# Kernel tuning notes

Measured on AMD Instinct MI355X. Metric: run time of the kernel, lower is better.

The kernel has to match this reference:

```python
import jax, jax.numpy as jnp
import numpy as np

B, DV, W, H = 128, 2048, 14, 14
S = W * H            # 196 spatial positions
DQ = 2048            # question vector dim
DA = 1200            # attention dim_v == dim_q == dim_mm (MLB elementwise fusion)
G = 4                # nb_glimpses
DH = 2048            # fusion dim_h (total); per-glimpse = DH // G
NANS = 3000


def setup_inputs() -> dict:
    key = jax.random.key(0)
    ks = jax.random.split(key, 16)
    s = 0.02
    return {
        "input_v": jax.random.normal(ks[0], (B, DV, W, H), jnp.float32),
        "x_q_vec": jax.random.normal(ks[1], (B, DQ), jnp.float32),
        # conv_v_att: 1x1 conv DV->DA  (expressed as channel matmul)
        "Wv_att": jax.random.normal(ks[2], (DV, DA), jnp.float32) * s,
        "bv_att": jnp.zeros((DA,), jnp.float32),
        # linear_q_att: DQ->DA
        "Wq_att": jax.random.normal(ks[3], (DQ, DA), jnp.float32) * s,
        "bq_att": jnp.zeros((DA,), jnp.float32),
        # conv_att: 1x1 conv DA->G
        "Wa": jax.random.normal(ks[4], (DA, G), jnp.float32) * s,
        "ba": jnp.zeros((G,), jnp.float32),
        # per-glimpse fusion linears DV -> DH//G, stacked over glimpses
        "Wf": jax.random.normal(ks[5], (G, DV, DH // G), jnp.float32) * s,
        "bf": jnp.zeros((G, DH // G), jnp.float32),
        # linear_q_fusion: DQ -> DH
        "Wqf": jax.random.normal(ks[6], (DQ, DH), jnp.float32) * s,
        "bqf": jnp.zeros((DH,), jnp.float32),
        # linear_classif: DH -> NANS
        "Wc": jax.random.normal(ks[7], (DH, NANS), jnp.float32) * s,
        "bc": jnp.zeros((NANS,), jnp.float32),
    }


def reference(input_v, x_q_vec, Wv_att, bv_att, Wq_att, bq_att, Wa, ba,
              Wf, bf, Wqf, bqf, Wc, bc):
    b = input_v.shape[0]
    v_flat = input_v.reshape(b, DV, S)                      # [B, DV, S]

    # --- attention scores ---
    # conv_v_att (1x1) + tanh -> [B, S, DA]
    x_v = jnp.tanh(jnp.einsum('bcs,cd->bsd', v_flat, Wv_att) + bv_att)
    # linear_q_att + tanh -> [B, DA], broadcast over spatial
    x_q = jnp.tanh(x_q_vec @ Wq_att + bq_att)
    # MLB fusion_att: elementwise multiply, then tanh (activation_mm)
    x_att = jnp.tanh(x_v * x_q[:, None, :])                 # [B, S, DA]
    scores = jnp.einsum('bsd,dg->bsg', x_att, Wa) + ba      # [B, S, G]
    att = jax.nn.softmax(scores, axis=1)                    # softmax over spatial

    # --- weighted pooling per glimpse ---
    v_att = jnp.einsum('bsg,bcs->bgc', att, v_flat)         # [B, G, DV]

    # --- fusion of glimpses ---
    xv = jnp.tanh(jnp.einsum('bgc,gch->bgh', v_att, Wf) + bf)  # [B, G, DH/G]
    xv = xv.reshape(b, DH)                                   # concat glimpses
    xq = jnp.tanh(x_q_vec @ Wqf + bqf)                       # [B, DH]
    x = xv * xq                                              # MLB fusion_classif

    # --- classifier ---
    x = jnp.tanh(x)
    return x @ Wc + bc                                       # [B, NANS]
```

## Files before the change

### kernel.cpp

```cpp
#include <hip/hip_runtime.h>
#include <hip/hip_bf16.h>

#define BB   128
#define DV   2048
#define SS   196
#define DQ   2048
#define DA   1200
#define DAP  1280
#define GG   4
#define DH   2048
#define NANS 3000
#define NANSP 3008
#define MROWS (BB*SS)
#define NT   10
#define KSPLIT 8
#define KCHUNK (DV/KSPLIT)
#define NQ   (DAP + DH)

typedef __attribute__((ext_vector_type(8))) short bf16x8;
typedef __attribute__((ext_vector_type(4))) float f32x4;

__device__ __forceinline__ float fast_tanh(float x) {
    float e = __expf(2.0f * x);
    return 1.0f - 2.0f * __builtin_amdgcn_rcpf(e + 1.0f);
}

__device__ __forceinline__ void async_copy16(const void* gsrc, void* ldst) {
    __builtin_amdgcn_global_load_lds(
        (const __attribute__((address_space(1))) void*)gsrc,
        (__attribute__((address_space(3))) void*)ldst, 16, 0, 0);
}

__global__ void pad_misc(const float* __restrict__ bv, const float* __restrict__ Wa,
                         float* __restrict__ bvp, float* __restrict__ wap) {
    int i = blockIdx.x * 256 + threadIdx.x;
    if (i < DAP) bvp[i] = (i < DA) ? bv[i] : 0.f;
    if (i < DAP * GG) {
        int d = i >> 2;
        wap[i] = (d < DA) ? Wa[i] : 0.f;
    }
}

__global__ __launch_bounds__(256) void transpose_v(const float* __restrict__ v,
                                                   __hip_bfloat16* __restrict__ vt) {
    __shared__ float tile[128][65];
    const int b  = blockIdx.z;
    const int c0 = blockIdx.x * 128;
    const int s0 = blockIdx.y * 64;
    const int t  = threadIdx.x;
    const int sl = t & 63;
    const int cr = t >> 6;
    const float* src = v + (size_t)b * DV * SS;
    const int sg = s0 + sl;
    const bool sok = sg < SS;
#pragma unroll
    for (int i = 0; i < 32; ++i) {
        int c = cr + i * 4;
        tile[c][sl] = sok ? src[(size_t)(c0 + c) * SS + sg] : 0.f;
    }
    __syncthreads();
    const int cp = (t & 63) * 2;
#pragma unroll
    for (int i = 0; i < 16; ++i) {
        int s = (t >> 6) + i * 4;
        int sgl = s0 + s;
        if (sgl < SS) {
            __hip_bfloat162 h2;
            h2.x = __float2bfloat16(tile[cp][s]);
            h2.y = __float2bfloat16(tile[cp + 1][s]);
            *(__hip_bfloat162*)(vt + ((size_t)b * SS + sgl) * DV + c0 + cp) = h2;
        }
    }
}

__global__ __launch_bounds__(256) void transpose_w(const float* __restrict__ Wv,
                                                   __hip_bfloat16* __restrict__ wvt) {
    __shared__ float tile[64][65];
    const int d0 = blockIdx.x * 64;
    const int c0 = blockIdx.y * 64;
    const int t  = threadIdx.x;
    const int col  = t & 63;
    const int rowb = t >> 6;
#pragma unroll
    for (int i = 0; i < 16; ++i) {
        int c = rowb + i * 4;
        int d = d0 + col;
        tile[c][col] = (d < DA) ? Wv[(size_t)(c0 + c) * DA + d] : 0.f;
    }
    __syncthreads();
#pragma unroll
    for (int i = 0; i < 16; ++i) {
        int dl = rowb + i * 4;
        wvt[(size_t)(d0 + dl) * DV + c0 + col] = __float2bfloat16(tile[col][dl]);
    }
}

template <int SEL>
__global__ __launch_bounds__(256) void gemm_partial(
    const float* __restrict__ A, int lda,
    const float* __restrict__ Bm, const float* __restrict__ B2,
    float* __restrict__ Cp, int Npad) {
    __shared__ float As[64 * 132];
    __shared__ float Bs[64 * 68];
    const int t     = threadIdx.x;
    const int n0    = blockIdx.x * 64;
    const int kbase = blockIdx.y * KCHUNK;

    const float* Aeff = A;
    const float* Beff;
    int ldb, ncol0, nlim;
    if (SEL == 0) {
        Beff = Bm; ldb = NANS; ncol0 = n0; nlim = NANS;
    } else if (SEL == 1) {
        int gg = n0 >> 9;
        Aeff = A + gg * 2048;
        Beff = Bm + (size_t)gg * 2048 * 512;
        ldb = 512; ncol0 = n0 & 511; nlim = 1 << 30;
    } else {
        if (n0 < DAP) { Beff = Bm; ldb = DA; ncol0 = n0;      nlim = DA; }
        else          { Beff = B2; ldb = DH; ncol0 = n0 - DAP; nlim = 1 << 30; }
    }

    const int tm = (t & 31) * 4;
    const int tn = (t >> 5) * 8;
    float acc[4][8] = {};

    for (int k0 = kbase; k0 < kbase + KCHUNK; k0 += 64) {
        {
            int kk = t & 63, mb = (t >> 6) * 32;
#pragma unroll
            for (int i = 0; i < 32; ++i)
                As[kk * 132 + mb + i] = Aeff[(size_t)(mb + i) * lda + k0 + kk];
        }
        {
            int j = t & 63, kr = t >> 6;
            bool ok = (ncol0 + j) < nlim;
#pragma unroll
            for (int i = 0; i < 16; ++i) {
                int k = kr + i * 4;
                Bs[k * 68 + j] = ok ? Beff[(size_t)(k0 + k) * ldb + ncol0 + j] : 0.f;
            }
        }
        __syncthreads();
#pragma unroll
        for (int kk = 0; kk < 64; ++kk) {
            const float4 av = *(const float4*)(As + kk * 132 + tm);
            const float4 b0 = *(const float4*)(Bs + kk * 68 + tn);
            const float4 b1 = *(const float4*)(Bs + kk * 68 + tn + 4);
            const float am[4] = {av.x, av.y, av.z, av.w};
#pragma unroll
            for (int i = 0; i < 4; ++i) {
                acc[i][0] += am[i] * b0.x; acc[i][1] += am[i] * b0.y;
                acc[i][2] += am[i] * b0.z; acc[i][3] += am[i] * b0.w;
                acc[i][4] += am[i] * b1.x; acc[i][5] += am[i] * b1.y;
                acc[i][6] += am[i] * b1.z; acc[i][7] += am[i] * b1.w;
            }
        }
        __syncthreads();
    }
#pragma unroll
    for (int i = 0; i < 4; ++i) {
        size_t base = ((size_t)blockIdx.y * 128 + tm + i) * Npad + n0 + tn;
        float4 v0 = {acc[i][0], acc[i][1], acc[i][2], acc[i][3]};
        float4 v1 = {acc[i][4], acc[i][5], acc[i][6], acc[i][7]};
        *(float4*)(Cp + base) = v0;
        *(float4*)(Cp + base + 4) = v1;
    }
}

template <int MODE>
__global__ __launch_bounds__(256) void gemm_epilogue(
    const float* __restrict__ Cp, int Npad, int Nreal,
    const float* __restrict__ bias, const float* __restrict__ aux,
    float* __restrict__ out, int ldo) {
    int n = blockIdx.x * 256 + threadIdx.x;
    int m = blockIdx.y;
    if (n >= Npad) return;
    float s = 0.f;
#pragma unroll
    for (int ks = 0; ks < KSPLIT; ++ks)
        s += Cp[((size_t)ks * 128 + m) * Npad + n];
    if (MODE == 0) {
        if (n >= Nreal) return;
        out[(size_t)m * ldo + n] = s + bias[n];
    } else {
        float xv = fast_tanh(s + bias[n]);
        out[(size_t)m * ldo + n] = fast_tanh(xv * aux[(size_t)m * 2048 + n]);
    }
}

__global__ __launch_bounds__(256) void epilogue_q(
    const float* __restrict__ Cp,
    const float* __restrict__ bqa, const float* __restrict__ bqf,
    float* __restrict__ qatt, float* __restrict__ qfus) {
    int n = blockIdx.x * 256 + threadIdx.x;
    int m = blockIdx.y;
    if (n >= NQ) return;
    float s = 0.f;
#pragma unroll
    for (int ks = 0; ks < KSPLIT; ++ks)
        s += Cp[((size_t)ks * 128 + m) * NQ + n];
    if (n < DAP) {
        qatt[(size_t)m * DAP + n] = (n < DA) ? fast_tanh(s + bqa[n]) : 0.f;
    } else {
        int j = n - DAP;
        qfus[(size_t)m * DH + j] = fast_tanh(s + bqf[j]);
    }
}

__global__ __launch_bounds__(256) void big_gemm(
    const __hip_bfloat16* __restrict__ vt,
    const __hip_bfloat16* __restrict__ wt,
    const float* __restrict__ bvp,
    const float* __restrict__ qatt,
    const float* __restrict__ wap,
    float* __restrict__ scores_p) {
    __shared__ __hip_bfloat16 As[128 * 64];
    __shared__ __hip_bfloat16 Bs[128 * 64];
    __shared__ float wa_s[128 * 4];
    __shared__ float sc[128 * 4];
    __shared__ float qs[2 * 128];
    const int t    = threadIdx.x;
    const int lane = t & 63;
    const int w    = t >> 6;
    const int wm   = w >> 1, wn = w & 1;

    int bid = blockIdx.x;
    int grp = bid / 80, r = bid % 80;
    int mt, nt;
    if (grp < 24) { mt = grp * 8 + (r & 7); nt = r >> 3; }
    else          { mt = 192 + (r & 3);     nt = r >> 2; }
    const int m0 = mt * 128, n0 = nt * 128;
    const int b0 = m0 / SS;
    const int b1 = (m0 + 127) / SS;
    const int bsplit = (b0 + 1) * SS;

    if (t < 128) {
        *(float4*)(wa_s + t * 4) = *(const float4*)(wap + (n0 + t) * 4);
        *(float4*)(sc + t * 4) = (float4){0.f, 0.f, 0.f, 0.f};
        qs[t]       = qatt[(size_t)b0 * DAP + n0 + t];
        qs[128 + t] = qatt[(size_t)b1 * DAP + n0 + t];
    }

    f32x4 acc[4][4];
#pragma unroll
    for (int i = 0; i < 4; ++i)
#pragma unroll
        for (int j = 0; j < 4; ++j) acc[i][j] = (f32x4){0.f, 0.f, 0.f, 0.f};

    const int srow   = lane >> 3;
    const int schunk = (lane & 7) ^ srow;
    const __hip_bfloat16* aG = vt + (size_t)(m0 + w * 32 + srow) * DV + schunk * 8;
    const __hip_bfloat16* bG = wt + (size_t)(n0 + w * 32 + srow) * DV + schunk * 8;
    __hip_bfloat16* aL = As + (w * 32) * 64;
    __hip_bfloat16* bL = Bs + (w * 32) * 64;

    for (int k0 = 0; k0 < DV; k0 += 64) {
        __syncthreads();
#pragma unroll
        for (int j = 0; j < 4; ++j) {
            async_copy16(aG + (size_t)(j * 8) * DV + k0, aL + j * 8 * 64);
            async_copy16(bG + (size_t)(j * 8) * DV + k0, bL + j * 8 * 64);
        }
        __syncthreads();
#pragma unroll
        for (int ks = 0; ks < 2; ++ks) {
            const int cx = ((ks * 4 + (lane >> 4)) ^ (lane & 7)) * 8;
            bf16x8 a[4], b[4];
#pragma unroll
            for (int mi = 0; mi < 4; ++mi)
                a[mi] = *(const bf16x8*)(As + (wm * 64 + mi * 16 + (lane & 15)) * 64 + cx);
#pragma unroll
            for (int ni = 0; ni < 4; ++ni)
                b[ni] = *(const bf16x8*)(Bs + (wn * 64 + ni * 16 + (lane & 15)) * 64 + cx);
#pragma unroll
            for (int mi = 0; mi < 4; ++mi)
#pragma unroll
                for (int ni = 0; ni < 4; ++ni)
                    acc[mi][ni] = __builtin_amdgcn_mfma_f32_16x16x32_bf16(a[mi], b[ni], acc[mi][ni], 0, 0, 0);
        }
    }

    const int colb_l = wn * 64 + (lane & 15);
    const int colb_g = n0 + colb_l;
    float bvv[4];
    float4 wv[4];
#pragma unroll
    for (int ni = 0; ni < 4; ++ni) {
        bvv[ni] = bvp[colb_g + ni * 16];
        wv[ni]  = *(const float4*)(wa_s + (colb_l + ni * 16) * 4);
    }
#pragma unroll
    for (int mi = 0; mi < 4; ++mi) {
#pragma unroll
        for (int rr = 0; rr < 4; ++rr) {
            int lrow = wm * 64 + mi * 16 + ((lane >> 4) << 2) + rr;
            int row  = m0 + lrow;
            int qoff = (row >= bsplit) ? 128 : 0;
            float p0 = 0.f, p1 = 0.f, p2 = 0.f, p3 = 0.f;
#pragma unroll
            for (int ni = 0; ni < 4; ++ni) {
                float xv = fast_tanh(acc[mi][ni][rr] + bvv[ni]);
                float xa = fast_tanh(xv * qs[qoff + colb_l + ni * 16]);
                p0 += xa * wv[ni].x; p1 += xa * wv[ni].y;
                p2 += xa * wv[ni].z; p3 += xa * wv[ni].w;
            }
#pragma unroll
            for (int mk = 1; mk < 16; mk <<= 1) {
                p0 += __shfl_xor(p0, mk); p1 += __shfl_xor(p1, mk);
                p2 += __shfl_xor(p2, mk); p3 += __shfl_xor(p3, mk);
            }
            if ((lane & 15) == 0) {
                atomicAdd(sc + lrow * 4 + 0, p0);
                atomicAdd(sc + lrow * 4 + 1, p1);
                atomicAdd(sc + lrow * 4 + 2, p2);
                atomicAdd(sc + lrow * 4 + 3, p3);
            }
        }
    }
    __syncthreads();
    if (t < 128)
        *(float4*)(scores_p + ((size_t)nt * MROWS + m0 + t) * 4) = *(float4*)(sc + t * 4);
}

__global__ __launch_bounds__(256) void softmax_pool(
    const float* __restrict__ scores_p,
    const __hip_bfloat16* __restrict__ vt,
    float* __restrict__ vatt) {
    __shared__ __align__(16) float att[SS * GG];
    const int b = blockIdx.y;
    const int t = threadIdx.x;
    if (t < SS) {
        float4 s = {0.f, 0.f, 0.f, 0.f};
#pragma unroll
        for (int ntile = 0; ntile < NT; ++ntile) {
            float4 p = *(const float4*)(scores_p + ((size_t)ntile * MROWS + b * SS + t) * 4);
            s.x += p.x; s.y += p.y; s.z += p.z; s.w += p.w;
        }
        *(float4*)(att + t * 4) = s;
    }
    __syncthreads();
    {
        const int g = t >> 6;
        const int lane = t & 63;
        float mx = -3.0e38f;
        for (int s = lane; s < SS; s += 64) mx = fmaxf(mx, att[s * 4 + g]);
#pragma unroll
        for (int m = 32; m > 0; m >>= 1) mx = fmaxf(mx, __shfl_xor(mx, m));
        float sum = 0.f;
        for (int s = lane; s < SS; s += 64) sum += __expf(att[s * 4 + g] - mx);
#pragma unroll
        for (int m = 32; m > 0; m >>= 1) sum += __shfl_xor(sum, m);
        float inv = __builtin_amdgcn_rcpf(sum);
        for (int s = lane; s < SS; s += 64) att[s * 4 + g] = __expf(att[s * 4 + g] - mx) * inv;
    }
    __syncthreads();
    const int c = blockIdx.x * 512 + t * 2;
    const __hip_bfloat16* vp = vt + (size_t)b * SS * DV + c;
    float a00 = 0, a01 = 0, a02 = 0, a03 = 0;
    float a10 = 0, a11 = 0, a12 = 0, a13 = 0;
#pragma unroll 4
    for (int s = 0; s < SS; ++s) {
        unsigned u = *(const unsigned*)(vp + (size_t)s * DV);
        float v0 = __uint_as_float(u << 16);
        float v1 = __uint_as_float(u & 0xffff0000u);
        float4 aw = *(const float4*)(att + s * 4);
        a00 += v0 * aw.x; a01 += v0 * aw.y; a02 += v0 * aw.z; a03 += v0 * aw.w;
        a10 += v1 * aw.x; a11 += v1 * aw.y; a12 += v1 * aw.z; a13 += v1 * aw.w;
    }
    float* vb = vatt + (size_t)b * GG * DV;
    vb[0 * DV + c] = a00; vb[0 * DV + c + 1] = a10;
    vb[1 * DV + c] = a01; vb[1 * DV + c + 1] = a11;
    vb[2 * DV + c] = a02; vb[2 * DV + c + 1] = a12;
    vb[3 * DV + c] = a03; vb[3 * DV + c + 1] = a13;
}

extern "C" void kernel_launch(void* const* d_in, const int* in_sizes, int n_in,
                              void* d_out, int out_size, void* d_ws, size_t ws_size,
                              hipStream_t stream) {
    const float* input_v = (const float*)d_in[0];
    const float* x_q     = (const float*)d_in[1];
    const float* Wv      = (const float*)d_in[2];
    const float* bv      = (const float*)d_in[3];
    const float* Wq_att  = (const float*)d_in[4];
    const float* bq_att  = (const float*)d_in[5];
    const float* Wa      = (const float*)d_in[6];
    const float* Wf      = (const float*)d_in[8];
    const float* bf_     = (const float*)d_in[9];
    const float* Wqf     = (const float*)d_in[10];
    const float* bqf     = (const float*)d_in[11];
    const float* Wc      = (const float*)d_in[12];
    const float* bc      = (const float*)d_in[13];
    float* out = (float*)d_out;

    char* wsb = (char*)d_ws;
    size_t off = 0;
    auto carve = [&](size_t bytes) -> void* {
        void* p = wsb + off;
        off += (bytes + 255) & ~(size_t)255;
        return p;
    };
    __hip_bfloat16* vt  = (__hip_bfloat16*)carve((size_t)MROWS * DV * 2);
    __hip_bfloat16* wvt = (__hip_bfloat16*)carve((size_t)DAP * DV * 2);
    float* Cp       = (float*)carve((size_t)KSPLIT * 128 * NQ * 4);
    float* scores_p = (float*)carve((size_t)NT * MROWS * GG * 4);
    float* qatt = (float*)carve((size_t)BB * DAP * 4);
    float* qfus = (float*)carve((size_t)BB * DH * 4);
    float* bvp  = (float*)carve((size_t)DAP * 4);
    float* wap  = (float*)carve((size_t)DAP * GG * 4);
    float* vatt = (float*)carve((size_t)BB * GG * DV * 4);
    float* xbuf = (float*)carve((size_t)BB * DH * 4);
    (void)ws_size; (void)n_in; (void)in_sizes; (void)out_size;

    pad_misc<<<dim3(20), 256, 0, stream>>>(bv, Wa, bvp, wap);
    transpose_v<<<dim3(DV / 128, 4, BB), 256, 0, stream>>>(input_v, vt);
    transpose_w<<<dim3(DAP / 64, DV / 64), 256, 0, stream>>>(Wv, wvt);

    gemm_partial<2><<<dim3(NQ / 64, KSPLIT), 256, 0, stream>>>(
        x_q, DQ, Wq_att, Wqf, Cp, NQ);
    epilogue_q<<<dim3(NQ / 256, BB), 256, 0, stream>>>(Cp, bq_att, bqf, qatt, qfus);

    big_gemm<<<dim3(24 * 80 + 40), 256, 0, stream>>>(vt, wvt, bvp, qatt, wap, scores_p);

    softmax_pool<<<dim3(4, BB), 256, 0, stream>>>(scores_p, vt, vatt);

    gemm_partial<1><<<dim3(DH / 64, KSPLIT), 256, 0, stream>>>(
        vatt, GG * DV, Wf, nullptr, Cp, DH);
    gemm_epilogue<2><<<dim3(DH / 256, BB), 256, 0, stream>>>(
        Cp, DH, DH, bf_, qfus, xbuf, DH);

    gemm_partial<0><<<dim3(NANSP / 64, KSPLIT), 256, 0, stream>>>(
        xbuf, DH, Wc, nullptr, Cp, NANSP);
    gemm_epilogue<0><<<dim3(NANSP / 256 + 1, BB), 256, 0, stream>>>(
        Cp, NANSP, NANS, bc, nullptr, out, NANS);
}
```

Before: 778.5 us.

## Enlarge big_gemm tiles to 256x256 with double-buffered async LDS loads

The main attention GEMM now computes 256x256 output tiles with 512-thread blocks instead of 128x128 tiles with 256 threads. Operand loads are double-buffered in 128KB of LDS, with vmcnt waits so the next k-slice's global-to-LDS copy overlaps the current MFMA work. The per-row score reduction writes per-wave partials to LDS and sums them, replacing LDS atomics. Fewer N tiles halves the partial-score buffer, but the large LDS footprint limits occupancy and the launch_bounds(512,2) hint may not be achievable.

```diff
diff --git a/kernel.cpp b/kernel.cpp
--- a/kernel.cpp
+++ b/kernel.cpp
@@ -12,7 +12,7 @@
 #define NANS 3000
 #define NANSP 3008
 #define MROWS (BB*SS)
-#define NT   10
+#define NT   5
 #define KSPLIT 8
 #define KCHUNK (DV/KSPLIT)
 #define NQ   (DAP + DH)
@@ -208,80 +208,108 @@
     }
 }
 
-__global__ __launch_bounds__(256) void big_gemm(
+__global__ __launch_bounds__(512, 2) void big_gemm(
     const __hip_bfloat16* __restrict__ vt,
     const __hip_bfloat16* __restrict__ wt,
     const float* __restrict__ bvp,
     const float* __restrict__ qatt,
     const float* __restrict__ wap,
     float* __restrict__ scores_p) {
-    __shared__ __hip_bfloat16 As[128 * 64];
-    __shared__ __hip_bfloat16 Bs[128 * 64];
-    __shared__ float wa_s[128 * 4];
-    __shared__ float sc[128 * 4];
-    __shared__ float qs[2 * 128];
+    __shared__ __align__(16) char lds[131072];
+    __shared__ __align__(16) float wa_s[256 * 4];
+    __shared__ float qs[3 * 256];
+
     const int t    = threadIdx.x;
     const int lane = t & 63;
     const int w    = t >> 6;
-    const int wm   = w >> 1, wn = w & 1;
+    const int wr   = w >> 2;
+    const int wc   = w & 3;
 
     int bid = blockIdx.x;
-    int grp = bid / 80, r = bid % 80;
+    int grp = bid / 40, r = bid % 40;
     int mt, nt;
-    if (grp < 24) { mt = grp * 8 + (r & 7); nt = r >> 3; }
-    else          { mt = 192 + (r & 3);     nt = r >> 2; }
-    const int m0 = mt * 128, n0 = nt * 128;
-    const int b0 = m0 / SS;
-    const int b1 = (m0 + 127) / SS;
-    const int bsplit = (b0 + 1) * SS;
-
-    if (t < 128) {
-        *(float4*)(wa_s + t * 4) = *(const float4*)(wap + (n0 + t) * 4);
-        *(float4*)(sc + t * 4) = (float4){0.f, 0.f, 0.f, 0.f};
-        qs[t]       = qatt[(size_t)b0 * DAP + n0 + t];
-        qs[128 + t] = qatt[(size_t)b1 * DAP + n0 + t];
-    }
-
-    f32x4 acc[4][4];
-#pragma unroll
-    for (int i = 0; i < 4; ++i)
-#pragma unroll
-        for (int j = 0; j < 4; ++j) acc[i][j] = (f32x4){0.f, 0.f, 0.f, 0.f};
+    if (grp < 12) { mt = grp * 8 + (r & 7); nt = r >> 3; }
+    else          { mt = 96 + (r & 1);      nt = r >> 1; }
+    const int m0 = mt * 256, n0 = nt * 256;
+    const int b_lo = m0 / SS;
+    const int bs1  = (b_lo + 1) * SS;
+    const int bs2  = (b_lo + 2) * SS;
+
+    if (t < 256) *(float4*)(wa_s + t * 4) = *(const float4*)(wap + (n0 + t) * 4);
+    {
+        int j = t >> 8, c = t & 255;
+        int b = b_lo + j;
+        qs[t] = (b < BB) ? qatt[(size_t)b * DAP + n0 + c] : 0.f;
+        if (t < 256) {
+            int b2 = b_lo + 2;
+            qs[512 + t] = (b2 < BB) ? qatt[(size_t)b2 * DAP + n0 + t] : 0.f;
+        }
+    }
 
     const int srow   = lane >> 3;
     const int schunk = (lane & 7) ^ srow;
-    const __hip_bfloat16* aG = vt + (size_t)(m0 + w * 32 + srow) * DV + schunk * 8;
-    const __hip_bfloat16* bG = wt + (size_t)(n0 + w * 32 + srow) * DV + schunk * 8;
-    __hip_bfloat16* aL = As + (w * 32) * 64;
-    __hip_bfloat16* bL = Bs + (w * 32) * 64;
-
-    for (int k0 = 0; k0 < DV; k0 += 64) {
-        __syncthreads();
+    const __hip_bfloat16* aG = vt + (size_t)(m0 + w * 8 + srow) * DV + schunk * 8;
+    const __hip_bfloat16* bG = wt + (size_t)(n0 + w * 8 + srow) * DV + schunk * 8;
+
+    auto STAGE = [&](int buf, int kk) {
+        char* aL = lds + buf * 65536 + w * 1024;
+        char* bL = aL + 32768;
 #pragma unroll
         for (int j = 0; j < 4; ++j) {
-            async_copy16(aG + (size_t)(j * 8) * DV + k0, aL + j * 8 * 64);
-            async_copy16(bG + (size_t)(j * 8) * DV + k0, bL + j * 8 * 64);
-        }
-        __syncthreads();
+            async_copy16(aG + (size_t)(j * 64) * DV + kk, aL + j * 8192);
+            async_copy16(bG + (size_t)(j * 64) * DV + kk, bL + j * 8192);
+        }
+    };
+
+    f32x4 acc[8][4];
+#pragma unroll
+    for (int i = 0; i < 8; ++i)
+#pragma unroll
+        for (int j = 0; j < 4; ++j) acc[i][j] = (f32x4){0.f, 0.f, 0.f, 0.f};
+
+    STAGE(0, 0);
+
+    for (int kt = 0; kt < 32; ++kt) {
+        const int cur = kt & 1;
+        __builtin_amdgcn_s_barrier();
+        if (kt < 31) {
+            STAGE(cur ^ 1, (kt + 1) * 64);
+            asm volatile("s_waitcnt vmcnt(8)" ::: "memory");
+        } else {
+            asm volatile("s_waitcnt vmcnt(0)" ::: "memory");
+        }
+        __builtin_amdgcn_s_barrier();
+
+        const __hip_bfloat16* As = (const __hip_bfloat16*)(lds + cur * 65536);
+        const __hip_bfloat16* Bs = As + 16384;
+        bf16x8 a[4], b[4];
 #pragma unroll
         for (int ks = 0; ks < 2; ++ks) {
             const int cx = ((ks * 4 + (lane >> 4)) ^ (lane & 7)) * 8;
-            bf16x8 a[4], b[4];
-#pragma unroll
-            for (int mi = 0; mi < 4; ++mi)
-                a[mi] = *(const bf16x8*)(As + (wm * 64 + mi * 16 + (lane & 15)) * 64 + cx);
 #pragma unroll
             for (int ni = 0; ni < 4; ++ni)
-                b[ni] = *(const bf16x8*)(Bs + (wn * 64 + ni * 16 + (lane & 15)) * 64 + cx);
-#pragma unroll
-            for (int mi = 0; mi < 4; ++mi)
-#pragma unroll
-                for (int ni = 0; ni < 4; ++ni)
-                    acc[mi][ni] = __builtin_amdgcn_mfma_f32_16x16x32_bf16(a[mi], b[ni], acc[mi][ni], 0, 0, 0);
-        }
-    }
-
-    const int colb_l = wn * 64 + (lane & 15);
+                b[ni] = *(const bf16x8*)(Bs + (wc * 64 + ni * 16 + (lane & 15)) * 64 + cx);
+#pragma unroll
+            for (int h = 0; h < 2; ++h) {
+#pragma unroll
+                for (int q = 0; q < 4; ++q)
+                    a[q] = *(const bf16x8*)(As + (wr * 128 + (h * 4 + q) * 16 + (lane & 15)) * 64 + cx);
+                __builtin_amdgcn_s_setprio(1);
+#pragma unroll
+                for (int q = 0; q < 4; ++q)
+#pragma unroll
+                    for (int ni = 0; ni < 4; ++ni)
+                        acc[h * 4 + q][ni] = __builtin_amdgcn_mfma_f32_16x16x32_bf16(
+                            a[q], b[ni], acc[h * 4 + q][ni], 0, 0, 0);
+                __builtin_amdgcn_s_setprio(0);
+            }
+        }
+    }
+
+    __syncthreads();
+    float* sc = (float*)lds;
+
+    const int colb_l = wc * 64 + (lane & 15);
     const int colb_g = n0 + colb_l;
     float bvv[4];
     float4 wv[4];
@@ -291,12 +319,12 @@
         wv[ni]  = *(const float4*)(wa_s + (colb_l + ni * 16) * 4);
     }
 #pragma unroll
-    for (int mi = 0; mi < 4; ++mi) {
+    for (int mi = 0; mi < 8; ++mi) {
 #pragma unroll
         for (int rr = 0; rr < 4; ++rr) {
-            int lrow = wm * 64 + mi * 16 + ((lane >> 4) << 2) + rr;
+            int lrow = wr * 128 + mi * 16 + ((lane >> 4) << 2) + rr;
             int row  = m0 + lrow;
-            int qoff = (row >= bsplit) ? 128 : 0;
+            int qoff = (row >= bs1 ? 256 : 0) + (row >= bs2 ? 256 : 0);
             float p0 = 0.f, p1 = 0.f, p2 = 0.f, p3 = 0.f;
 #pragma unroll
             for (int ni = 0; ni < 4; ++ni) {
@@ -310,17 +338,21 @@
                 p0 += __shfl_xor(p0, mk); p1 += __shfl_xor(p1, mk);
                 p2 += __shfl_xor(p2, mk); p3 += __shfl_xor(p3, mk);
             }
-            if ((lane & 15) == 0) {
-                atomicAdd(sc + lrow * 4 + 0, p0);
-                atomicAdd(sc + lrow * 4 + 1, p1);
-                atomicAdd(sc + lrow * 4 + 2, p2);
-                atomicAdd(sc + lrow * 4 + 3, p3);
-            }
-        }
-    }
-    __syncthreads();
-    if (t < 128)
-        *(float4*)(scores_p + ((size_t)nt * MROWS + m0 + t) * 4) = *(float4*)(sc + t * 4);
+            if ((lane & 15) == 0)
+                *(float4*)(sc + ((size_t)wc * 256 + lrow) * 4) =
+                    (float4){p0, p1, p2, p3};
+        }
+    }
+    __syncthreads();
+    if (t < 256) {
+        float4 s0 = *(float4*)(sc + (0 * 256 + t) * 4);
+        float4 s1 = *(float4*)(sc + (1 * 256 + t) * 4);
+        float4 s2 = *(float4*)(sc + (2 * 256 + t) * 4);
+        float4 s3 = *(float4*)(sc + (3 * 256 + t) * 4);
+        float4 s = {s0.x + s1.x + s2.x + s3.x, s0.y + s1.y + s2.y + s3.y,
+                    s0.z + s1.z + s2.z + s3.z, s0.w + s1.w + s2.w + s3.w};
+        *(float4*)(scores_p + ((size_t)nt * MROWS + m0 + t) * 4) = s;
+    }
 }
 
 __global__ __launch_bounds__(256) void softmax_pool(
@@ -420,7 +452,7 @@
         x_q, DQ, Wq_att, Wqf, Cp, NQ);
     epilogue_q<<<dim3(NQ / 256, BB), 256, 0, stream>>>(Cp, bq_att, bqf, qatt, qfus);
 
-    big_gemm<<<dim3(24 * 80 + 40), 256, 0, stream>>>(vt, wvt, bvp, qatt, wap, scores_p);
+    big_gemm<<<dim3(490), 512, 0, stream>>>(vt, wvt, bvp, qatt, wap, scores_p);
 
     softmax_pool<<<dim3(4, BB), 256, 0, stream>>>(scores_p, vt, vatt);
 
```

Result: no change. 764.4 us (-1.8%).
